# Performance work log

Hardware: AMD Instinct MI355X
Metric: run time of the kernel (lower is better)

## Reference

```python
import jax, jax.numpy as jnp
import numpy as np
from jax import lax

B, F_A, F_S, H, T = 4096, 64, 256, 1024, 64
DT = 0.05


def setup_inputs() -> dict:
    key = jax.random.key(0)
    k1, k2, k3, k4, k5, k6 = jax.random.split(key, 6)
    scale1 = 1.0 / np.sqrt(F_A + F_S)
    scale2 = 1.0 / np.sqrt(H)
    return {
        "ts": jnp.arange(T, dtype=jnp.float32) * DT,
        "actions": jax.random.normal(k1, (B, F_A, T), dtype=jnp.float32),
        "y0": jax.random.normal(k2, (B, F_S), dtype=jnp.float32),
        "W1": jax.random.normal(k3, (F_A + F_S, H), dtype=jnp.float32) * scale1,
        "b1": jnp.zeros((H,), dtype=jnp.float32),
        "W2": jax.random.normal(k4, (H, F_S), dtype=jnp.float32) * scale2,
        "b2": jnp.zeros((F_S,), dtype=jnp.float32),
        "dt": jnp.float32(DT),
    }


def reference(ts, actions, y0, W1, b1, W2, b2, dt):
    # ODEFunc: f(cat([a, y], -1)) with 2-layer tanh MLP; Euler: y' = y + dt*f
    def f(a, y):
        s = jnp.concatenate([a, y], axis=-1)        # (B, F_a+F_s)
        h = jnp.tanh(s @ W1 + b1)                   # (B, H)
        return h @ W2 + b2                          # (B, F_s)

    acts_t = jnp.transpose(actions, (2, 0, 1))      # (T, B, F_a)

    def step(y, a):
        y_next = y + dt * f(a, y)
        return y_next, y_next

    # y(ts[0]) = y0; T-1 euler steps driven by actions at times 0..T-2
    _, ys = lax.scan(step, y0, acts_t[:-1])         # (T-1, B, F_s)
    traj = jnp.concatenate([y0[None], ys], axis=0)  # (T, B, F_s)
    return jnp.transpose(traj, (1, 2, 0))           # (B, F_s, T)
```

## Files before the change

kernel.cpp:

```cpp
#include <hip/hip_runtime.h>

typedef _Float16 v8h __attribute__((ext_vector_type(8)));
typedef float v4f __attribute__((ext_vector_type(4)));

#define NT 512
#define XSTR 344
#define HSTR 1032

static constexpr size_t ATT_BYTES_NEEDED = 2359296ull + 4096ull * 64 * 64 * 4;

#define MFMA16 __builtin_amdgcn_mfma_f32_16x16x32_f16

#define GLOAD(dst, base, vo) \
  asm volatile("global_load_dwordx4 %0, %1, %2" : "=v"(dst) : "v"(vo), "s"(base))
#define VMW_(n) asm volatile("s_waitcnt vmcnt(" #n ")" ::: "memory")
#define VMW(n) do { VMW_(n); __builtin_amdgcn_sched_barrier(0); } while (0)
#define LGKMBAR() do { asm volatile("s_waitcnt lgkmcnt(0)" ::: "memory"); \
  __builtin_amdgcn_s_barrier(); } while (0)

__device__ __forceinline__ float tanh_fast(float a) {
  float e = __expf(2.0f * a);
  return 1.0f - __fdividef(2.0f, e + 1.0f);
}

extern "C" __global__ void conv_w(const float* __restrict__ W1,
                                  const float* __restrict__ W2,
                                  _Float16* __restrict__ ws) {
  int i = blockIdx.x * 256 + threadIdx.x;
  if (i < 327680) {
    int j = i & 7, lane = (i >> 3) & 63, w = (i >> 9) & 7, gp = i >> 12;
    int g = lane >> 4, l15 = lane & 15;
    int ph = gp / 10, p = gp % 10;
    float v = W1[(p * 32 + g * 8 + j) * 1024 + ph * 128 + w * 16 + l15];
    _Float16 hh = (_Float16)v;
    ws[i] = hh;
    ws[327680 + i] = (_Float16)((v - (float)hh) * 2048.f);
  } else {
    int iq = i - 655360;
    if (iq >= 0) {
      int j = iq & 7, t = (iq >> 3) & 511, s = iq >> 12;
      int lane = t & 63, wave = t >> 6, g = lane >> 4, l15 = lane & 15;
      int p = s >> 1, ph2 = s & 1;
      float v = W2[(p * 32 + g * 8 + j) * 256 + ph2 * 128 + wave * 16 + l15];
      _Float16 hh = (_Float16)v;
      ws[655360 + iq] = hh;
      ws[917504 + iq] = (_Float16)((v - (float)hh) * 2048.f);
    }
  }
}

extern "C" __global__ void conv_a(const float* __restrict__ actions,
                                  float* __restrict__ att) {
  size_t o = (size_t)blockIdx.x * 256 + threadIdx.x;
  int f = (int)(o & 63);
  int b = (int)((o >> 6) & 4095);
  int t = (int)(o >> 18);
  att[o] = actions[((size_t)b * 64 + f) * 64 + t];
}

#define G1BODY(p, RF, N, RD0) do { \
    VMW(N); \
    v8h bh = B1H[(p) % 5], bl = B1L[(p) % 5]; \
    if (RF) { GLOAD(B1H[(p) % 5], w1hB, vo1); GLOAD(B1L[(p) % 5], w1lB, vo1); \
              vo1 += 8192; } \
    v8h xch = Xh[(p) & 1], xcl = Xl[(p) & 1]; \
    if ((p) < 9) { \
      Xh[((p) + 1) & 1] = *(const v8h*)&xHs[xbase + ((p) + 1) * 32]; \
      Xl[((p) + 1) & 1] = *(const v8h*)&xLs[xbase + ((p) + 1) * 32]; \
    } else if (RD0) { \
      Xh[0] = *(const v8h*)&xHs[xbase]; \
      Xl[0] = *(const v8h*)&xLs[xbase]; \
    } \
    accH = MFMA16(xch, bh, accH, 0, 0, 0); \
    accM = MFMA16(xch, bl, accM, 0, 0, 0); \
    accM = MFMA16(xcl, bh, accM, 0, 0, 0); \
  } while (0)

#define G2BODY(j, s3, par, RF, N) do { \
    VMW(N); \
    v8h bh0 = B2H0[s3], bl0 = B2L0[s3]; \
    v8h bh1 = B2H1[s3], bl1 = B2L1[s3]; \
    if (RF) { \
      GLOAD(B2H0[s3], w2hB, vo2); GLOAD(B2L0[s3], w2lB, vo2); \
      GLOAD(B2H1[s3], w2hB, vo2 + 8192); GLOAD(B2L1[s3], w2lB, vo2 + 8192); \
      vo2 += 16384; \
    } \
    v8h hch = Hh[par], hcl = Hl_[par]; \
    if ((j) < 31) { \
      Hh[(par) ^ 1] = *(const v8h*)&hHs[hbase + ((j) + 1) * 32]; \
      Hl_[(par) ^ 1] = *(const v8h*)&hLs[hbase + ((j) + 1) * 32]; \
    } \
    c0H = MFMA16(hch, bh0, c0H, 0, 0, 0); \
    c0M = MFMA16(hch, bl0, c0M, 0, 0, 0); \
    c0M = MFMA16(hcl, bh0, c0M, 0, 0, 0); \
    c1H = MFMA16(hch, bh1, c1H, 0, 0, 0); \
    c1M = MFMA16(hch, bl1, c1M, 0, 0, 0); \
    c1M = MFMA16(hcl, bh1, c1M, 0, 0, 0); \
  } while (0)

extern "C" __global__ void __launch_bounds__(NT, 2)
ode_kernel(const float* __restrict__ actions, const float* __restrict__ att,
           const float* __restrict__ y0,
           const float* __restrict__ b1f, const float* __restrict__ b2f,
           const float* __restrict__ dtp, const _Float16* __restrict__ ws,
           float* __restrict__ out)
{
  __shared__ __align__(16) _Float16 xHs[16 * XSTR], xLs[16 * XSTR];
  __shared__ __align__(16) _Float16 hHs[16 * HSTR], hLs[16 * HSTR];
  __shared__ float b1s[1024];

  const int tid  = threadIdx.x;
  const int lane = tid & 63;
  const int l15  = lane & 15, g = lane >> 4;
  const int nloc = (tid >> 6) * 16 + l15;
  const int b0   = blockIdx.x * 16;
  const float dt = dtp[0];
  const int tid16 = tid * 16;

  const _Float16* w1hB = ws;
  const _Float16* w1lB = ws + 327680;
  const _Float16* w2hB = ws + 655360;
  const _Float16* w2lB = ws + 917504;

  for (int i = tid; i < 1024; i += NT) b1s[i] = b1f[i];
  const float b2r0 = b2f[nloc], b2r1 = b2f[128 + nloc];

  float ya[4], yb[4];
  #pragma unroll
  for (int j = 0; j < 4; ++j) {
    int m = g * 4 + j;
    ya[j] = y0[(size_t)(b0 + m) * 256 + nloc];
    yb[j] = y0[(size_t)(b0 + m) * 256 + 128 + nloc];
    out[((size_t)((b0 + m) * 256 + nloc)) * 64] = ya[j];
    out[((size_t)((b0 + m) * 256 + 128 + nloc)) * 64] = yb[j];
  }

  const int xbase = l15 * XSTR + g * 8;
  const int hbase = l15 * HSTR + g * 8;

  v8h B1H[5], B1L[5];
  v8h B2H0[3], B2L0[3], B2H1[3], B2L1[3];
  v8h Xh[2], Xl[2], Hh[2], Hl_[2];

  #pragma unroll
  for (int s = 0; s < 5; ++s) {
    GLOAD(B1H[s], w1hB, tid16 + s * 8192);
    GLOAD(B1L[s], w1lB, tid16 + s * 8192);
  }

  #pragma unroll 1
  for (int t = 0; t < 63; ++t) {
    #pragma unroll
    for (int it = 0; it < 2; ++it) {
      int o = tid + NT * it;
      int m = o >> 6, k = o & 63;
      float v = att ? att[((size_t)t * 4096 + b0 + m) * 64 + k]
                    : actions[((size_t)(b0 + m) * 64 + k) * 64 + t];
      _Float16 hh = (_Float16)v;
      xHs[m * XSTR + k] = hh;
      xLs[m * XSTR + k] = (_Float16)((v - (float)hh) * 2048.f);
    }
    #pragma unroll
    for (int j = 0; j < 4; ++j) {
      int m = g * 4 + j;
      _Float16 h0 = (_Float16)ya[j];
      xHs[m * XSTR + 64 + nloc] = h0;
      xLs[m * XSTR + 64 + nloc] = (_Float16)((ya[j] - (float)h0) * 2048.f);
      _Float16 h1 = (_Float16)yb[j];
      xHs[m * XSTR + 192 + nloc] = h1;
      xLs[m * XSTR + 192 + nloc] = (_Float16)((yb[j] - (float)h1) * 2048.f);
    }
    LGKMBAR();

    Xh[0] = *(const v8h*)&xHs[xbase];
    Xl[0] = *(const v8h*)&xLs[xbase];

    int vo1 = tid16 + 5 * 8192;

    #pragma unroll 1
    for (int ph = 0; ph < 7; ++ph) {
      const float bb = b1s[ph * 128 + nloc];
      v4f accH = v4f{bb, bb, bb, bb};
      v4f accM = v4f{0.f, 0.f, 0.f, 0.f};
      #pragma unroll
      for (int p = 0; p < 10; ++p) G1BODY(p, 1, 8, 1);
      #pragma unroll
      for (int j = 0; j < 4; ++j) {
        float v = accH[j] + accM[j] * (1.f / 2048.f);
        float th = tanh_fast(v);
        _Float16 hh = (_Float16)th;
        int m = g * 4 + j;
        hHs[m * HSTR + ph * 128 + nloc] = hh;
        hLs[m * HSTR + ph * 128 + nloc] = (_Float16)((th - (float)hh) * 2048.f);
      }
    }
    {
      const float bb = b1s[7 * 128 + nloc];
      v4f accH = v4f{bb, bb, bb, bb};
      v4f accM = v4f{0.f, 0.f, 0.f, 0.f};
      #pragma unroll
      for (int p = 0; p < 6; ++p) G1BODY(p, (p) < 5, 8, 1);
      G1BODY(6, 0, 6, 1);
      GLOAD(B2H0[0], w2hB, tid16);          GLOAD(B2L0[0], w2lB, tid16);
      GLOAD(B2H1[0], w2hB, tid16 + 8192);   GLOAD(B2L1[0], w2lB, tid16 + 8192);
      G1BODY(7, 0, 8, 1);
      GLOAD(B2H0[1], w2hB, tid16 + 16384);  GLOAD(B2L0[1], w2lB, tid16 + 16384);
      GLOAD(B2H1[1], w2hB, tid16 + 24576);  GLOAD(B2L1[1], w2lB, tid16 + 24576);
      G1BODY(8, 0, 10, 1);
      GLOAD(B2H0[2], w2hB, tid16 + 32768);  GLOAD(B2L0[2], w2lB, tid16 + 32768);
      GLOAD(B2H1[2], w2hB, tid16 + 40960);  GLOAD(B2L1[2], w2lB, tid16 + 40960);
      G1BODY(9, 0, 12, 0);
      #pragma unroll
      for (int j = 0; j < 4; ++j) {
        float v = accH[j] + accM[j] * (1.f / 2048.f);
        float th = tanh_fast(v);
        _Float16 hh = (_Float16)th;
        int m = g * 4 + j;
        hHs[m * HSTR + 7 * 128 + nloc] = hh;
        hLs[m * HSTR + 7 * 128 + nloc] = (_Float16)((th - (float)hh) * 2048.f);
      }
    }
    LGKMBAR();

    Hh[0] = *(const v8h*)&hHs[hbase];
    Hl_[0] = *(const v8h*)&hLs[hbase];

    int vo2 = tid16 + 3 * 16384;

    v4f c0H = v4f{b2r0, b2r0, b2r0, b2r0}, c0M = v4f{0.f, 0.f, 0.f, 0.f};
    v4f c1H = v4f{b2r1, b2r1, b2r1, b2r1}, c1M = v4f{0.f, 0.f, 0.f, 0.f};

    #pragma unroll 1
    for (int jj = 0; jj < 4; ++jj) {
      const int jb = jj * 6;
      G2BODY(jb + 0, 0, 0, 1, 8);
      G2BODY(jb + 1, 1, 1, 1, 8);
      G2BODY(jb + 2, 2, 0, 1, 8);
      G2BODY(jb + 3, 0, 1, 1, 8);
      G2BODY(jb + 4, 1, 0, 1, 8);
      G2BODY(jb + 5, 2, 1, 1, 8);
    }
    G2BODY(24, 0, 0, 1, 8);
    G2BODY(25, 1, 1, 1, 8);
    G2BODY(26, 2, 0, 1, 8);
    G2BODY(27, 0, 1, 1, 8);
    G2BODY(28, 1, 0, 1, 8);
    G2BODY(29, 2, 1, 0, 8);
    G2BODY(30, 0, 0, 0, 4);
    G2BODY(31, 1, 1, 0, 0);

    #pragma unroll
    for (int j = 0; j < 4; ++j) {
      int m = g * 4 + j;
      float yn0 = ya[j] + dt * (c0H[j] + c0M[j] * (1.f / 2048.f));
      ya[j] = yn0;
      out[((size_t)((b0 + m) * 256 + nloc)) * 64 + (t + 1)] = yn0;
      float yn1 = yb[j] + dt * (c1H[j] + c1M[j] * (1.f / 2048.f));
      yb[j] = yn1;
      out[((size_t)((b0 + m) * 256 + 128 + nloc)) * 64 + (t + 1)] = yn1;
    }
    if (t < 62) {
      #pragma unroll
      for (int s = 0; s < 5; ++s) {
        GLOAD(B1H[s], w1hB, tid16 + s * 8192);
        GLOAD(B1L[s], w1lB, tid16 + s * 8192);
      }
    }
  }
}

extern "C" void kernel_launch(void* const* d_in, const int* in_sizes, int n_in,
                              void* d_out, int out_size, void* d_ws, size_t ws_size,
                              hipStream_t stream) {
  const float* actions = (const float*)d_in[1];
  const float* y0      = (const float*)d_in[2];
  const float* W1      = (const float*)d_in[3];
  const float* b1      = (const float*)d_in[4];
  const float* W2      = (const float*)d_in[5];
  const float* b2      = (const float*)d_in[6];
  const float* dtp     = (const float*)d_in[7];
  float* out = (float*)d_out;
  _Float16* ws = (_Float16*)d_ws;

  const bool use_att = ws_size >= ATT_BYTES_NEEDED;
  float* att = use_att ? (float*)((char*)d_ws + 2359296) : nullptr;

  hipLaunchKernelGGL(conv_w, dim3(3584), dim3(256), 0, stream, W1, W2, ws);
  if (use_att)
    hipLaunchKernelGGL(conv_a, dim3(65536), dim3(256), 0, stream, actions, att);
  hipLaunchKernelGGL(ode_kernel, dim3(256), dim3(NT), 0, stream,
                     actions, att, y0, b1, b2, dtp, ws, out);
}
```

Measured before the change: 2.335 ms.

## Double block size to 1024 threads and rework weight tiling per wave

Raises the thread block from 512 to 1024 threads (16 waves), so each wave owns 16 output columns of a 256-wide slice. The weight pre-swizzle and the software-pipelined global loads are rewritten to match. Layer 1 now runs in two passes of two accumulator pairs, and layer 2 uses a single accumulator pair per wave. This halves per-thread register and accumulator pressure and drops the LDS bias table, but removes the two-blocks-per-CU launch bound and shortens the prefetch depth.

After: 2.607 ms. 11.7% more time.

```diff
diff --git a/kernel.cpp b/kernel.cpp
--- a/kernel.cpp
+++ b/kernel.cpp
@@ -3,7 +3,7 @@
 typedef _Float16 v8h __attribute__((ext_vector_type(8)));
 typedef float v4f __attribute__((ext_vector_type(4)));
 
-#define NT 512
+#define NT 1024
 #define XSTR 344
 #define HSTR 1032
 
@@ -28,20 +28,20 @@
                                   _Float16* __restrict__ ws) {
   int i = blockIdx.x * 256 + threadIdx.x;
   if (i < 327680) {
-    int j = i & 7, lane = (i >> 3) & 63, w = (i >> 9) & 7, gp = i >> 12;
-    int g = lane >> 4, l15 = lane & 15;
-    int ph = gp / 10, p = gp % 10;
-    float v = W1[(p * 32 + g * 8 + j) * 1024 + ph * 128 + w * 16 + l15];
+    int jj = i & 7, tid = (i >> 3) & 1023, s = i >> 13;
+    int w = tid >> 6, g = (tid >> 4) & 3, l15 = tid & 15;
+    int a = s / 20, r = s % 20, p = r >> 1, u = r & 1;
+    int col = (a * 2 + u) * 256 + w * 16 + l15;
+    float v = W1[(p * 32 + g * 8 + jj) * 1024 + col];
     _Float16 hh = (_Float16)v;
     ws[i] = hh;
     ws[327680 + i] = (_Float16)((v - (float)hh) * 2048.f);
   } else {
     int iq = i - 655360;
     if (iq >= 0) {
-      int j = iq & 7, t = (iq >> 3) & 511, s = iq >> 12;
-      int lane = t & 63, wave = t >> 6, g = lane >> 4, l15 = lane & 15;
-      int p = s >> 1, ph2 = s & 1;
-      float v = W2[(p * 32 + g * 8 + j) * 256 + ph2 * 128 + wave * 16 + l15];
+      int jj = iq & 7, tid = (iq >> 3) & 1023, q = iq >> 13;
+      int w = tid >> 6, g = (tid >> 4) & 3, l15 = tid & 15;
+      float v = W2[(q * 32 + g * 8 + jj) * 256 + w * 16 + l15];
       _Float16 hh = (_Float16)v;
       ws[655360 + iq] = hh;
       ws[917504 + iq] = (_Float16)((v - (float)hh) * 2048.f);
@@ -58,47 +58,59 @@
   att[o] = actions[((size_t)b * 64 + f) * 64 + t];
 }
 
-#define G1BODY(p, RF, N, RD0) do { \
+#define G1BODY(p, RF, N, PF0) do { \
     VMW(N); \
-    v8h bh = B1H[(p) % 5], bl = B1L[(p) % 5]; \
-    if (RF) { GLOAD(B1H[(p) % 5], w1hB, vo1); GLOAD(B1L[(p) % 5], w1lB, vo1); \
-              vo1 += 8192; } \
+    v8h bh0 = B1H0[(p) & 1], bl0 = B1L0[(p) & 1]; \
+    v8h bh1 = B1H1[(p) & 1], bl1 = B1L1[(p) & 1]; \
+    if (RF) { \
+      GLOAD(B1H0[(p) & 1], w1hB, vo1); GLOAD(B1L0[(p) & 1], w1lB, vo1); \
+      GLOAD(B1H1[(p) & 1], w1hB, vo1 + 16384); \
+      GLOAD(B1L1[(p) & 1], w1lB, vo1 + 16384); \
+      vo1 += 32768; } \
     v8h xch = Xh[(p) & 1], xcl = Xl[(p) & 1]; \
     if ((p) < 9) { \
       Xh[((p) + 1) & 1] = *(const v8h*)&xHs[xbase + ((p) + 1) * 32]; \
       Xl[((p) + 1) & 1] = *(const v8h*)&xLs[xbase + ((p) + 1) * 32]; \
-    } else if (RD0) { \
+    } else if (PF0) { \
       Xh[0] = *(const v8h*)&xHs[xbase]; \
       Xl[0] = *(const v8h*)&xLs[xbase]; \
     } \
-    accH = MFMA16(xch, bh, accH, 0, 0, 0); \
-    accM = MFMA16(xch, bl, accM, 0, 0, 0); \
-    accM = MFMA16(xcl, bh, accM, 0, 0, 0); \
-  } while (0)
-
-#define G2BODY(j, s3, par, RF, N) do { \
+    acc0H = MFMA16(xch, bh0, acc0H, 0, 0, 0); \
+    acc0M = MFMA16(xch, bl0, acc0M, 0, 0, 0); \
+    acc0M = MFMA16(xcl, bh0, acc0M, 0, 0, 0); \
+    acc1H = MFMA16(xch, bh1, acc1H, 0, 0, 0); \
+    acc1M = MFMA16(xch, bl1, acc1M, 0, 0, 0); \
+    acc1M = MFMA16(xcl, bh1, acc1M, 0, 0, 0); \
+  } while (0)
+
+#define B1PRO(sl, s0) do { \
+    GLOAD(B1H0[sl], w1hB, tid16 + (s0) * 16384); \
+    GLOAD(B1L0[sl], w1lB, tid16 + (s0) * 16384); \
+    GLOAD(B1H1[sl], w1hB, tid16 + ((s0) + 1) * 16384); \
+    GLOAD(B1L1[sl], w1lB, tid16 + ((s0) + 1) * 16384); \
+  } while (0)
+
+#define B2PRO3() do { \
+    GLOAD(B2H[0], w2hB, tid16);          GLOAD(B2L[0], w2lB, tid16); \
+    GLOAD(B2H[1], w2hB, tid16 + 16384);  GLOAD(B2L[1], w2lB, tid16 + 16384); \
+    GLOAD(B2H[2], w2hB, tid16 + 32768);  GLOAD(B2L[2], w2lB, tid16 + 32768); \
+  } while (0)
+
+#define G2BODY(s3, par, RF, RD, N, nxt) do { \
     VMW(N); \
-    v8h bh0 = B2H0[s3], bl0 = B2L0[s3]; \
-    v8h bh1 = B2H1[s3], bl1 = B2L1[s3]; \
-    if (RF) { \
-      GLOAD(B2H0[s3], w2hB, vo2); GLOAD(B2L0[s3], w2lB, vo2); \
-      GLOAD(B2H1[s3], w2hB, vo2 + 8192); GLOAD(B2L1[s3], w2lB, vo2 + 8192); \
-      vo2 += 16384; \
-    } \
+    v8h bh = B2H[s3], bl = B2L[s3]; \
+    if (RF) { GLOAD(B2H[s3], w2hB, vo2); GLOAD(B2L[s3], w2lB, vo2); \
+              vo2 += 16384; } \
     v8h hch = Hh[par], hcl = Hl_[par]; \
-    if ((j) < 31) { \
-      Hh[(par) ^ 1] = *(const v8h*)&hHs[hbase + ((j) + 1) * 32]; \
-      Hl_[(par) ^ 1] = *(const v8h*)&hLs[hbase + ((j) + 1) * 32]; \
-    } \
-    c0H = MFMA16(hch, bh0, c0H, 0, 0, 0); \
-    c0M = MFMA16(hch, bl0, c0M, 0, 0, 0); \
-    c0M = MFMA16(hcl, bh0, c0M, 0, 0, 0); \
-    c1H = MFMA16(hch, bh1, c1H, 0, 0, 0); \
-    c1M = MFMA16(hch, bl1, c1M, 0, 0, 0); \
-    c1M = MFMA16(hcl, bh1, c1M, 0, 0, 0); \
-  } while (0)
-
-extern "C" __global__ void __launch_bounds__(NT, 2)
+    if (RD) { \
+      Hh[(par) ^ 1]  = *(const v8h*)&hHs[hbase + (nxt)]; \
+      Hl_[(par) ^ 1] = *(const v8h*)&hLs[hbase + (nxt)]; } \
+    cH = MFMA16(hch, bh, cH, 0, 0, 0); \
+    cM = MFMA16(hch, bl, cM, 0, 0, 0); \
+    cM = MFMA16(hcl, bh, cM, 0, 0, 0); \
+  } while (0)
+
+extern "C" __global__ void __launch_bounds__(NT)
 ode_kernel(const float* __restrict__ actions, const float* __restrict__ att,
            const float* __restrict__ y0,
            const float* __restrict__ b1f, const float* __restrict__ b2f,
@@ -107,12 +119,12 @@
 {
   __shared__ __align__(16) _Float16 xHs[16 * XSTR], xLs[16 * XSTR];
   __shared__ __align__(16) _Float16 hHs[16 * HSTR], hLs[16 * HSTR];
-  __shared__ float b1s[1024];
 
   const int tid  = threadIdx.x;
   const int lane = tid & 63;
   const int l15  = lane & 15, g = lane >> 4;
-  const int nloc = (tid >> 6) * 16 + l15;
+  const int w    = tid >> 6;
+  const int nl   = w * 16 + l15;
   const int b0   = blockIdx.x * 16;
   const float dt = dtp[0];
   const int tid16 = tid * 16;
@@ -122,38 +134,31 @@
   const _Float16* w2hB = ws + 655360;
   const _Float16* w2lB = ws + 917504;
 
-  for (int i = tid; i < 1024; i += NT) b1s[i] = b1f[i];
-  const float b2r0 = b2f[nloc], b2r1 = b2f[128 + nloc];
-
-  float ya[4], yb[4];
+  float b1r[4];
   #pragma unroll
-  for (int j = 0; j < 4; ++j) {
-    int m = g * 4 + j;
-    ya[j] = y0[(size_t)(b0 + m) * 256 + nloc];
-    yb[j] = y0[(size_t)(b0 + m) * 256 + 128 + nloc];
-    out[((size_t)((b0 + m) * 256 + nloc)) * 64] = ya[j];
-    out[((size_t)((b0 + m) * 256 + 128 + nloc)) * 64] = yb[j];
+  for (int j = 0; j < 4; ++j) b1r[j] = b1f[j * 256 + nl];
+  const float b2r = b2f[nl];
+
+  float ya[4];
+  #pragma unroll
+  for (int r = 0; r < 4; ++r) {
+    ya[r] = y0[(size_t)(b0 + g * 4 + r) * 256 + nl];
+    out[((size_t)((b0 + g * 4 + r) * 256 + nl)) * 64] = ya[r];
   }
 
   const int xbase = l15 * XSTR + g * 8;
   const int hbase = l15 * HSTR + g * 8;
 
-  v8h B1H[5], B1L[5];
-  v8h B2H0[3], B2L0[3], B2H1[3], B2L1[3];
+  v8h B1H0[2], B1L0[2], B1H1[2], B1L1[2];
+  v8h B2H[3], B2L[3];
   v8h Xh[2], Xl[2], Hh[2], Hl_[2];
 
-  #pragma unroll
-  for (int s = 0; s < 5; ++s) {
-    GLOAD(B1H[s], w1hB, tid16 + s * 8192);
-    GLOAD(B1L[s], w1lB, tid16 + s * 8192);
-  }
+  B1PRO(0, 0); B1PRO(1, 2);
 
   #pragma unroll 1
   for (int t = 0; t < 63; ++t) {
-    #pragma unroll
-    for (int it = 0; it < 2; ++it) {
-      int o = tid + NT * it;
-      int m = o >> 6, k = o & 63;
+    {
+      int m = tid >> 6, k = tid & 63;
       float v = att ? att[((size_t)t * 4096 + b0 + m) * 64 + k]
                     : actions[((size_t)(b0 + m) * 64 + k) * 64 + t];
       _Float16 hh = (_Float16)v;
@@ -161,111 +166,104 @@
       xLs[m * XSTR + k] = (_Float16)((v - (float)hh) * 2048.f);
     }
     #pragma unroll
-    for (int j = 0; j < 4; ++j) {
-      int m = g * 4 + j;
-      _Float16 h0 = (_Float16)ya[j];
-      xHs[m * XSTR + 64 + nloc] = h0;
-      xLs[m * XSTR + 64 + nloc] = (_Float16)((ya[j] - (float)h0) * 2048.f);
-      _Float16 h1 = (_Float16)yb[j];
-      xHs[m * XSTR + 192 + nloc] = h1;
-      xLs[m * XSTR + 192 + nloc] = (_Float16)((yb[j] - (float)h1) * 2048.f);
+    for (int r = 0; r < 4; ++r) {
+      int m = g * 4 + r;
+      _Float16 h0 = (_Float16)ya[r];
+      xHs[m * XSTR + 64 + nl] = h0;
+      xLs[m * XSTR + 64 + nl] = (_Float16)((ya[r] - (float)h0) * 2048.f);
     }
     LGKMBAR();
 
     Xh[0] = *(const v8h*)&xHs[xbase];
     Xl[0] = *(const v8h*)&xLs[xbase];
 
-    int vo1 = tid16 + 5 * 8192;
-
-    #pragma unroll 1
-    for (int ph = 0; ph < 7; ++ph) {
-      const float bb = b1s[ph * 128 + nloc];
-      v4f accH = v4f{bb, bb, bb, bb};
-      v4f accM = v4f{0.f, 0.f, 0.f, 0.f};
+    int vo1 = tid16 + 4 * 16384;
+    {
+      v4f acc0H = v4f{b1r[0], b1r[0], b1r[0], b1r[0]};
+      v4f acc1H = v4f{b1r[1], b1r[1], b1r[1], b1r[1]};
+      v4f acc0M = v4f{0.f, 0.f, 0.f, 0.f}, acc1M = acc0M;
+      G1BODY(0, 1, 4, 0); G1BODY(1, 1, 4, 0); G1BODY(2, 1, 4, 0);
+      G1BODY(3, 1, 4, 0); G1BODY(4, 1, 4, 0); G1BODY(5, 1, 4, 0);
+      G1BODY(6, 1, 4, 0); G1BODY(7, 1, 4, 0);
+      G1BODY(8, 0, 4, 0); B1PRO(0, 20);
+      G1BODY(9, 0, 4, 1); B1PRO(1, 22);
       #pragma unroll
-      for (int p = 0; p < 10; ++p) G1BODY(p, 1, 8, 1);
+      for (int r = 0; r < 4; ++r) {
+        int m = g * 4 + r;
+        float v0 = acc0H[r] + acc0M[r] * (1.f / 2048.f);
+        float t0 = tanh_fast(v0);
+        _Float16 e0 = (_Float16)t0;
+        hHs[m * HSTR + nl] = e0;
+        hLs[m * HSTR + nl] = (_Float16)((t0 - (float)e0) * 2048.f);
+        float v1 = acc1H[r] + acc1M[r] * (1.f / 2048.f);
+        float t1 = tanh_fast(v1);
+        _Float16 e1 = (_Float16)t1;
+        hHs[m * HSTR + 256 + nl] = e1;
+        hLs[m * HSTR + 256 + nl] = (_Float16)((t1 - (float)e1) * 2048.f);
+      }
+    }
+    vo1 = tid16 + 24 * 16384;
+    {
+      v4f acc0H = v4f{b1r[2], b1r[2], b1r[2], b1r[2]};
+      v4f acc1H = v4f{b1r[3], b1r[3], b1r[3], b1r[3]};
+      v4f acc0M = v4f{0.f, 0.f, 0.f, 0.f}, acc1M = acc0M;
+      G1BODY(0, 1, 4, 0); G1BODY(1, 1, 4, 0); G1BODY(2, 1, 4, 0);
+      G1BODY(3, 1, 4, 0); G1BODY(4, 1, 4, 0); G1BODY(5, 1, 4, 0);
+      G1BODY(6, 1, 4, 0); G1BODY(7, 1, 4, 0);
+      G1BODY(8, 0, 4, 0);
+      G1BODY(9, 0, 0, 0);
+      B2PRO3();
       #pragma unroll
-      for (int j = 0; j < 4; ++j) {
-        float v = accH[j] + accM[j] * (1.f / 2048.f);
-        float th = tanh_fast(v);
-        _Float16 hh = (_Float16)th;
-        int m = g * 4 + j;
-        hHs[m * HSTR + ph * 128 + nloc] = hh;
-        hLs[m * HSTR + ph * 128 + nloc] = (_Float16)((th - (float)hh) * 2048.f);
+      for (int r = 0; r < 4; ++r) {
+        int m = g * 4 + r;
+        float v0 = acc0H[r] + acc0M[r] * (1.f / 2048.f);
+        float t0 = tanh_fast(v0);
+        _Float16 e0 = (_Float16)t0;
+        hHs[m * HSTR + 512 + nl] = e0;
+        hLs[m * HSTR + 512 + nl] = (_Float16)((t0 - (float)e0) * 2048.f);
+        float v1 = acc1H[r] + acc1M[r] * (1.f / 2048.f);
+        float t1 = tanh_fast(v1);
+        _Float16 e1 = (_Float16)t1;
+        hHs[m * HSTR + 768 + nl] = e1;
+        hLs[m * HSTR + 768 + nl] = (_Float16)((t1 - (float)e1) * 2048.f);
       }
     }
-    {
-      const float bb = b1s[7 * 128 + nloc];
-      v4f accH = v4f{bb, bb, bb, bb};
-      v4f accM = v4f{0.f, 0.f, 0.f, 0.f};
-      #pragma unroll
-      for (int p = 0; p < 6; ++p) G1BODY(p, (p) < 5, 8, 1);
-      G1BODY(6, 0, 6, 1);
-      GLOAD(B2H0[0], w2hB, tid16);          GLOAD(B2L0[0], w2lB, tid16);
-      GLOAD(B2H1[0], w2hB, tid16 + 8192);   GLOAD(B2L1[0], w2lB, tid16 + 8192);
-      G1BODY(7, 0, 8, 1);
-      GLOAD(B2H0[1], w2hB, tid16 + 16384);  GLOAD(B2L0[1], w2lB, tid16 + 16384);
-      GLOAD(B2H1[1], w2hB, tid16 + 24576);  GLOAD(B2L1[1], w2lB, tid16 + 24576);
-      G1BODY(8, 0, 10, 1);
-      GLOAD(B2H0[2], w2hB, tid16 + 32768);  GLOAD(B2L0[2], w2lB, tid16 + 32768);
-      GLOAD(B2H1[2], w2hB, tid16 + 40960);  GLOAD(B2L1[2], w2lB, tid16 + 40960);
-      G1BODY(9, 0, 12, 0);
-      #pragma unroll
-      for (int j = 0; j < 4; ++j) {
-        float v = accH[j] + accM[j] * (1.f / 2048.f);
-        float th = tanh_fast(v);
-        _Float16 hh = (_Float16)th;
-        int m = g * 4 + j;
-        hHs[m * HSTR + 7 * 128 + nloc] = hh;
-        hLs[m * HSTR + 7 * 128 + nloc] = (_Float16)((th - (float)hh) * 2048.f);
-      }
-    }
     LGKMBAR();
 
-    Hh[0] = *(const v8h*)&hHs[hbase];
+    Hh[0]  = *(const v8h*)&hHs[hbase];
     Hl_[0] = *(const v8h*)&hLs[hbase];
 
     int vo2 = tid16 + 3 * 16384;
 
-    v4f c0H = v4f{b2r0, b2r0, b2r0, b2r0}, c0M = v4f{0.f, 0.f, 0.f, 0.f};
-    v4f c1H = v4f{b2r1, b2r1, b2r1, b2r1}, c1M = v4f{0.f, 0.f, 0.f, 0.f};
+    v4f cH = v4f{b2r, b2r, b2r, b2r};
+    v4f cM = v4f{0.f, 0.f, 0.f, 0.f};
 
     #pragma unroll 1
     for (int jj = 0; jj < 4; ++jj) {
-      const int jb = jj * 6;
-      G2BODY(jb + 0, 0, 0, 1, 8);
-      G2BODY(jb + 1, 1, 1, 1, 8);
-      G2BODY(jb + 2, 2, 0, 1, 8);
-      G2BODY(jb + 3, 0, 1, 1, 8);
-      G2BODY(jb + 4, 1, 0, 1, 8);
-      G2BODY(jb + 5, 2, 1, 1, 8);
-    }
-    G2BODY(24, 0, 0, 1, 8);
-    G2BODY(25, 1, 1, 1, 8);
-    G2BODY(26, 2, 0, 1, 8);
-    G2BODY(27, 0, 1, 1, 8);
-    G2BODY(28, 1, 0, 1, 8);
-    G2BODY(29, 2, 1, 0, 8);
-    G2BODY(30, 0, 0, 0, 4);
-    G2BODY(31, 1, 1, 0, 0);
+      const int jb = jj * 192;
+      G2BODY(0, 0, 1, 1, 4, jb + 32);
+      G2BODY(1, 1, 1, 1, 4, jb + 64);
+      G2BODY(2, 0, 1, 1, 4, jb + 96);
+      G2BODY(0, 1, 1, 1, 4, jb + 128);
+      G2BODY(1, 0, 1, 1, 4, jb + 160);
+      G2BODY(2, 1, 1, 1, 4, jb + 192);
+    }
+    G2BODY(0, 0, 1, 1, 4, 800);
+    G2BODY(1, 1, 1, 1, 4, 832);
+    G2BODY(2, 0, 1, 1, 4, 864);
+    G2BODY(0, 1, 1, 1, 4, 896);
+    G2BODY(1, 0, 1, 1, 4, 928);
+    G2BODY(2, 1, 0, 1, 4, 960);
+    G2BODY(0, 0, 0, 1, 2, 992);
+    G2BODY(1, 1, 0, 0, 0, 0);
 
     #pragma unroll
-    for (int j = 0; j < 4; ++j) {
-      int m = g * 4 + j;
-      float yn0 = ya[j] + dt * (c0H[j] + c0M[j] * (1.f / 2048.f));
-      ya[j] = yn0;
-      out[((size_t)((b0 + m) * 256 + nloc)) * 64 + (t + 1)] = yn0;
-      float yn1 = yb[j] + dt * (c1H[j] + c1M[j] * (1.f / 2048.f));
-      yb[j] = yn1;
-      out[((size_t)((b0 + m) * 256 + 128 + nloc)) * 64 + (t + 1)] = yn1;
-    }
-    if (t < 62) {
-      #pragma unroll
-      for (int s = 0; s < 5; ++s) {
-        GLOAD(B1H[s], w1hB, tid16 + s * 8192);
-        GLOAD(B1L[s], w1lB, tid16 + s * 8192);
-      }
-    }
+    for (int r = 0; r < 4; ++r) {
+      float yn = ya[r] + dt * (cH[r] + cM[r] * (1.f / 2048.f));
+      ya[r] = yn;
+      out[((size_t)((b0 + g * 4 + r) * 256 + nl)) * 64 + (t + 1)] = yn;
+    }
+    if (t < 62) { B1PRO(0, 0); B1PRO(1, 2); }
   }
 }
 
```
